# Performance work log

Measured on AMD Instinct MI355X. Metric: run time of the kernel, lower is better.

Reference implementation:

```python
import jax, jax.numpy as jnp
import numpy as np

B, N, D = 8, 2048, 256      # batch, tokens, model dim (= out_token_dims)
S = 128                     # query_key_dims
H = int(2.0 * D)            # expansion_factor * D = 512
EPS = 1e-5


def setup_inputs() -> dict:
    key = jax.random.key(0)
    ks = jax.random.split(key, 4)
    x = jax.random.normal(ks[0], (B, N, D), dtype=jnp.float32)
    g = jnp.ones((), jnp.float32)                                # ScaleNorm gain
    W_uv = jax.random.normal(ks[1], (D, 2 * H + S), jnp.float32) * 0.02
    b_uv = jnp.zeros((2 * H + S,), jnp.float32)
    gamma = jnp.ones((2, S), jnp.float32)                        # OffsetScale scale
    beta = jnp.zeros((2, S), jnp.float32)                        # OffsetScale offset
    W_o = jax.random.normal(ks[2], (H, D), jnp.float32) * 0.02
    b_o = jnp.zeros((D,), jnp.float32)
    return {"x": x, "g": g, "W_uv": W_uv, "b_uv": b_uv,
            "gamma": gamma, "beta": beta, "W_o": W_o, "b_o": b_o}


def reference(x, g, W_uv, b_uv, gamma, beta, W_o, b_o):
    d = x.shape[-1]
    # ScaleNorm: x / max(||x|| / sqrt(d), eps) * g
    norm = jnp.linalg.norm(x, axis=-1, keepdims=True) * jax.lax.rsqrt(jnp.float32(d))
    xn = x / jnp.maximum(norm, EPS) * g
    # fused uv projection + SiLU
    uv = jax.nn.silu(jnp.einsum('bnd,de->bne', xn, W_uv) + b_uv)
    u = uv[..., :H]            # gate branch        [B,N,H]
    v = uv[..., H:2 * H]       # value branch       [B,N,H]
    base = uv[..., 2 * H:]     # shared q/k base    [B,N,S]
    # OffsetScale heads=2 -> q, k (cheap per-dim affine)
    q = base * gamma[0] + beta[0]
    k = base * gamma[1] + beta[1]
    # single-head scores + ReLU^2 attention activation
    qk = jnp.einsum('bns,bms->bnm', q, k) * jax.lax.rsqrt(jnp.float32(S))
    attn = jnp.square(jax.nn.relu(qk))
    # gate * (attn @ v), then output projection back to D
    gated = u * jnp.einsum('bnm,bmh->bnh', attn, v)
    return jnp.einsum('bnh,hd->bnd', gated, W_o) + b_o
```

## Files before the change

### kernel.cpp

```cpp
#include <hip/hip_runtime.h>
#include <math.h>

#define BB 8
#define NN 2048
#define DD 256
#define SS 128
#define HH 512
#define EE 1152

typedef short bf16x8 __attribute__((ext_vector_type(8)));
typedef float f32x4 __attribute__((ext_vector_type(4)));

__device__ __forceinline__ short f2bf(float f) {
    union { float f; unsigned u; } a; a.f = f;
    unsigned r = a.u + 0x7FFFu + ((a.u >> 16) & 1u);
    return (short)(r >> 16);
}
__device__ __forceinline__ float bf2f(short s) {
    union { unsigned u; float f; } a; a.u = ((unsigned)(unsigned short)s) << 16;
    return a.f;
}
__device__ __forceinline__ void gl_lds16(const short* g, short* l) {
    __builtin_amdgcn_global_load_lds(
        (const __attribute__((address_space(1))) void*)g,
        (__attribute__((address_space(3))) void*)l, 16, 0, 0);
}

__global__ __launch_bounds__(256) void k_pre(
        const float* __restrict__ x, const float* __restrict__ gp,
        short* __restrict__ xn,
        const float* __restrict__ Wuv, const float* __restrict__ Wo,
        short* __restrict__ Wuv_t, short* __restrict__ Wo_t) {
    __shared__ float tile[32][33];
    int bid = blockIdx.x;
    int t = threadIdx.x;
    if (bid < 4096) {
        int wave = t >> 6, lane = t & 63;
        long row = (long)bid * 4 + wave;
        float4 xv = ((const float4*)(x + row * DD))[lane];
        float ss = xv.x*xv.x + xv.y*xv.y + xv.z*xv.z + xv.w*xv.w;
        #pragma unroll
        for (int off = 32; off > 0; off >>= 1) ss += __shfl_down(ss, off);
        ss = __shfl(ss, 0);
        float norm = sqrtf(ss) * 0.0625f;
        float scale = gp[0] / fmaxf(norm, 1e-5f);
        short4 o;
        o.x = f2bf(xv.x * scale); o.y = f2bf(xv.y * scale);
        o.z = f2bf(xv.z * scale); o.w = f2bf(xv.w * scale);
        ((short4*)(xn + row * DD))[lane] = o;
    } else if (bid < 4384) {
        int bid2 = bid - 4096;
        int et = bid2 % 36, dt = bid2 / 36;
        #pragma unroll
        for (int i = 0; i < 4; i++) {
            int idx = t + i*256, r = idx >> 5, c = idx & 31;
            tile[r][c] = Wuv[(long)(dt*32 + r)*EE + et*32 + c];
        }
        __syncthreads();
        #pragma unroll
        for (int i = 0; i < 4; i++) {
            int idx = t + i*256, r = idx >> 5, c = idx & 31;
            Wuv_t[(long)(et*32 + r)*DD + dt*32 + c] = f2bf(tile[c][r]);
        }
    } else {
        int bid3 = bid - 4384;
        int ht = bid3 % 16, dt = bid3 / 16;
        #pragma unroll
        for (int i = 0; i < 4; i++) {
            int idx = t + i*256, r = idx >> 5, c = idx & 31;
            tile[r][c] = Wo[(long)(ht*32 + r)*DD + dt*32 + c];
        }
        __syncthreads();
        #pragma unroll
        for (int i = 0; i < 4; i++) {
            int idx = t + i*256, r = idx >> 5, c = idx & 31;
            Wo_t[(long)(dt*32 + r)*HH + ht*32 + c] = f2bf(tile[c][r]);
        }
    }
}

__global__ __launch_bounds__(256) void k_gemm1(
        const short* __restrict__ xn, const short* __restrict__ Wuv_t,
        const float* __restrict__ b_uv,
        const float* __restrict__ gamma, const float* __restrict__ beta,
        short* __restrict__ u, short* __restrict__ vfrag,
        short* __restrict__ q, short* __restrict__ k) {
    __shared__ short As[128*64];
    __shared__ short Bs[128*64];
    int m0 = blockIdx.x * 128, n0 = blockIdx.y * 128;
    int t = threadIdx.x, w = t >> 6, lane = t & 63;
    int wr = w & 1, wc = w >> 1, l16 = lane & 15, quad = lane >> 4;
    int lr = lane >> 3, lc = (lane & 7) * 8;
    f32x4 acc[4][4] = {};
    for (int k0 = 0; k0 < DD; k0 += 64) {
        __syncthreads();
        #pragma unroll
        for (int i = 0; i < 4; i++) {
            int r0 = i*32 + w*8;
            gl_lds16(&xn[(long)(m0 + r0 + lr)*DD + k0 + lc], &As[r0*64]);
            gl_lds16(&Wuv_t[(long)(n0 + r0 + lr)*DD + k0 + lc], &Bs[r0*64]);
        }
        __syncthreads();
        #pragma unroll
        for (int kk = 0; kk < 2; kk++) {
            bf16x8 a[4], bb[4];
            #pragma unroll
            for (int mt = 0; mt < 4; mt++)
                a[mt] = *(const bf16x8*)&As[(wr*64 + mt*16 + l16)*64 + kk*32 + quad*8];
            #pragma unroll
            for (int nt = 0; nt < 4; nt++)
                bb[nt] = *(const bf16x8*)&Bs[(wc*64 + nt*16 + l16)*64 + kk*32 + quad*8];
            #pragma unroll
            for (int mt = 0; mt < 4; mt++)
                #pragma unroll
                for (int nt = 0; nt < 4; nt++)
                    acc[mt][nt] = __builtin_amdgcn_mfma_f32_16x16x32_bf16(
                        a[mt], bb[nt], acc[mt][nt], 0,0,0);
        }
    }
    #pragma unroll
    for (int mt = 0; mt < 4; mt++)
    #pragma unroll
    for (int nt = 0; nt < 4; nt++) {
        int gm0 = m0 + wr*64 + mt*16 + quad*4;
        int ge  = n0 + wc*64 + nt*16 + l16;
        float val[4];
        #pragma unroll
        for (int r = 0; r < 4; r++) {
            float xv = acc[mt][nt][r] + b_uv[ge];
            val[r] = xv / (1.0f + __expf(-xv));
        }
        if (ge < HH) {
            #pragma unroll
            for (int r = 0; r < 4; r++)
                u[(long)(gm0 + r)*HH + ge] = f2bf(val[r]);
        } else if (ge < 2*HH) {
            int h = ge - HH;
            long base = (((long)((gm0 >> 11)*64 + ((gm0 & 2047) >> 5)) * 32)
                         + (h >> 4)) * 512
                        + ((((gm0 & 31) >> 3)*16 + (h & 15)) * 8) + (gm0 & 7);
            short4 o;
            o.x = f2bf(val[0]); o.y = f2bf(val[1]);
            o.z = f2bf(val[2]); o.w = f2bf(val[3]);
            *(short4*)&vfrag[base] = o;
        } else {
            int si = ge - 2*HH;
            #pragma unroll
            for (int r = 0; r < 4; r++) {
                q[(long)(gm0 + r)*SS + si] = f2bf(val[r] * gamma[si]      + beta[si]);
                k[(long)(gm0 + r)*SS + si] = f2bf(val[r] * gamma[SS + si] + beta[SS + si]);
            }
        }
    }
}

#define KS(p,row)  (smem + ((p)*32 + (row))*136)
#define PS(p,row)  (smem + 8704 + ((p)*64 + (row))*40)
#define GT(hf,row) (smem + (hf)*16896 + (row)*264)

__global__ __launch_bounds__(512, 2) void k_attn(
        const short* __restrict__ q, const short* __restrict__ k,
        const short* __restrict__ vfrag, const short* __restrict__ u,
        const short* __restrict__ Wo_t, const float* __restrict__ b_o,
        float* __restrict__ out) {
    extern __shared__ __align__(16) short smem[];
    int b = blockIdx.x & 7;
    int i0 = (blockIdx.x >> 3) * 64;
    int t = threadIdx.x, w = t >> 6, lane = t & 63;
    int l16 = lane & 15, quad = lane >> 4;
    int qt = w >> 1, mt = w & 1;
    const short* qb  = q + ((long)b * NN + i0) * SS;
    const short* kb  = k + (long)b * NN * SS;
    const short* vfb = vfrag + (long)b * 64 * 32 * 512;
    const float RS = 0.08838834764831845f;

    int krow = t >> 4, kch = (t & 15) * 8;

    bf16x8 qf[4];
    #pragma unroll
    for (int kc = 0; kc < 4; kc++)
        qf[kc] = *(const bf16x8*)&qb[(long)(qt*16 + l16)*SS + kc*32 + quad*8];

    *(bf16x8*)&KS(0,krow)[kch] = *(const bf16x8*)&kb[(long)krow*SS + kch];
    bf16x8 kpre = *(const bf16x8*)&kb[(long)(32 + krow)*SS + kch];
    __syncthreads();

    f32x4 acc[16] = {};
    for (int it = 0; it < NN/32; it++) {
        int p = it & 1;
        int m0 = it * 32;
        int mnext = (m0 + 64 < NN) ? m0 + 64 : m0;
        bf16x8 knext = *(const bf16x8*)&kb[(long)(mnext + krow)*SS + kch];
        bf16x8 vf[4];
        #pragma unroll
        for (int jj = 0; jj < 4; jj++)
            vf[jj] = *(const bf16x8*)&vfb[((long)it*32 + (w*4 + jj))*512 + lane*8];
        f32x4 sc = {};
        #pragma unroll
        for (int kc = 0; kc < 4; kc++) {
            bf16x8 kf = *(const bf16x8*)&KS(p, mt*16 + l16)[kc*32 + quad*8];
            sc = __builtin_amdgcn_mfma_f32_16x16x32_bf16(kf, qf[kc], sc, 0,0,0);
        }
        short4 pw;
        {
            float s0 = fmaxf(sc[0]*RS, 0.f), s1 = fmaxf(sc[1]*RS, 0.f);
            float s2 = fmaxf(sc[2]*RS, 0.f), s3 = fmaxf(sc[3]*RS, 0.f);
            pw.x = f2bf(s0*s0); pw.y = f2bf(s1*s1);
            pw.z = f2bf(s2*s2); pw.w = f2bf(s3*s3);
        }
        *(short4*)&PS(p, qt*16 + l16)[mt*16 + quad*4] = pw;
        *(bf16x8*)&KS(p^1, krow)[kch] = kpre;
        kpre = knext;
        __syncthreads();
        bf16x8 af[4];
        #pragma unroll
        for (int qq2 = 0; qq2 < 4; qq2++)
            af[qq2] = *(const bf16x8*)&PS(p, qq2*16 + l16)[quad*8];
        #pragma unroll
        for (int jj = 0; jj < 4; jj++)
            #pragma unroll
            for (int qq2 = 0; qq2 < 4; qq2++)
                acc[qq2*4 + jj] = __builtin_amdgcn_mfma_f32_16x16x32_bf16(
                    af[qq2], vf[jj], acc[qq2*4 + jj], 0,0,0);
    }

    long rowbase = (long)b * NN + i0;
    __syncthreads();
    {
        int hf = w >> 2;
        int hbase = (w & 3) * 64;
        #pragma unroll
        for (int qq2 = 0; qq2 < 4; qq2++)
        #pragma unroll
        for (int jj = 0; jj < 4; jj++) {
            int gh = w*64 + jj*16 + l16;
            #pragma unroll
            for (int r = 0; r < 4; r++) {
                long grow = rowbase + qq2*16 + quad*4 + r;
                float uval = bf2f(u[grow*HH + gh]);
                GT(hf, qq2*16 + quad*4 + r)[hbase + jj*16 + l16] =
                    f2bf(acc[qq2*4 + jj][r] * uval);
            }
        }
    }
    __syncthreads();
    f32x4 acc2[4][2] = {};
    #pragma unroll
    for (int p = 0; p < 2; p++) {
        #pragma unroll
        for (int kc = 0; kc < 8; kc++) {
            bf16x8 A[4], Bf[2];
            #pragma unroll
            for (int mt2 = 0; mt2 < 4; mt2++)
                A[mt2] = *(const bf16x8*)&GT(p, mt2*16 + l16)[kc*32 + quad*8];
            #pragma unroll
            for (int nt = 0; nt < 2; nt++)
                Bf[nt] = *(const bf16x8*)&Wo_t[(long)(w*32 + nt*16 + l16)*HH
                                               + p*256 + kc*32 + quad*8];
            #pragma unroll
            for (int mt2 = 0; mt2 < 4; mt2++)
                #pragma unroll
                for (int nt = 0; nt < 2; nt++)
                    acc2[mt2][nt] = __builtin_amdgcn_mfma_f32_16x16x32_bf16(
                        A[mt2], Bf[nt], acc2[mt2][nt], 0,0,0);
        }
    }
    #pragma unroll
    for (int mt2 = 0; mt2 < 4; mt2++)
    #pragma unroll
    for (int nt = 0; nt < 2; nt++)
    #pragma unroll
    for (int r = 0; r < 4; r++) {
        long grow = rowbase + mt2*16 + quad*4 + r;
        int gd = w*32 + nt*16 + l16;
        out[grow*DD + gd] = acc2[mt2][nt][r] + b_o[gd];
    }
}

extern "C" void kernel_launch(void* const* d_in, const int* in_sizes, int n_in,
                              void* d_out, int out_size, void* d_ws, size_t ws_size,
                              hipStream_t stream) {
    const float* x     = (const float*)d_in[0];
    const float* g     = (const float*)d_in[1];
    const float* Wuv   = (const float*)d_in[2];
    const float* b_uv  = (const float*)d_in[3];
    const float* gamma = (const float*)d_in[4];
    const float* beta  = (const float*)d_in[5];
    const float* Wo    = (const float*)d_in[6];
    const float* b_o   = (const float*)d_in[7];
    float* out = (float*)d_out;

    short* ws    = (short*)d_ws;
    short* xn    = ws;
    short* Wuv_t = xn    + (long)16384 * 256;
    short* Wo_t  = Wuv_t + (long)1152 * 256;
    short* u     = Wo_t  + (long)256 * 512;
    short* vfrag = u     + (long)16384 * 512;
    short* qq    = vfrag + (long)16384 * 512;
    short* kk    = qq    + (long)16384 * 128;

    k_pre<<<4512, 256, 0, stream>>>(x, g, xn, Wuv, Wo, Wuv_t, Wo_t);
    k_gemm1<<<dim3(128, 9), 256, 0, stream>>>(xn, Wuv_t, b_uv, gamma, beta,
                                              u, vfrag, qq, kk);
    k_attn<<<256, 512, 67584, stream>>>(qq, kk, vfrag, u, Wo_t, b_o, out);
}
```

Measured before the change: 163.7 us.

## Register-prefetch GEMM1 tiles and deepen attention K/V prefetch pipeline

GEMM1 now loads its A/B tiles with register prefetch: the next k-slice is fetched into registers while MFMAs run on the current one, replacing direct global-to-LDS loads. It also adds a launch-bounds occupancy hint. The attention loop is unrolled by two with ping-pong K buffers, and V fragments are loaded one stage earlier so global latency overlaps the MFMA work. The cost is higher register pressure, which could lower occupancy or cause spills.

```diff
diff --git a/kernel.cpp b/kernel.cpp
--- a/kernel.cpp
+++ b/kernel.cpp
@@ -19,11 +19,6 @@
 __device__ __forceinline__ float bf2f(short s) {
     union { unsigned u; float f; } a; a.u = ((unsigned)(unsigned short)s) << 16;
     return a.f;
-}
-__device__ __forceinline__ void gl_lds16(const short* g, short* l) {
-    __builtin_amdgcn_global_load_lds(
-        (const __attribute__((address_space(1))) void*)g,
-        (__attribute__((address_space(3))) void*)l, 16, 0, 0);
 }
 
 __global__ __launch_bounds__(256) void k_pre(
@@ -79,7 +74,7 @@
     }
 }
 
-__global__ __launch_bounds__(256) void k_gemm1(
+__global__ __launch_bounds__(256, 3) void k_gemm1(
         const short* __restrict__ xn, const short* __restrict__ Wuv_t,
         const float* __restrict__ b_uv,
         const float* __restrict__ gamma, const float* __restrict__ beta,
@@ -90,17 +85,29 @@
     int m0 = blockIdx.x * 128, n0 = blockIdx.y * 128;
     int t = threadIdx.x, w = t >> 6, lane = t & 63;
     int wr = w & 1, wc = w >> 1, l16 = lane & 15, quad = lane >> 4;
-    int lr = lane >> 3, lc = (lane & 7) * 8;
+    int srow = t >> 1, scol = (t & 1) * 32;
     f32x4 acc[4][4] = {};
-    for (int k0 = 0; k0 < DD; k0 += 64) {
+    bf16x8 aS[4], bS[4];
+    #pragma unroll
+    for (int j = 0; j < 4; j++) {
+        aS[j] = *(const bf16x8*)&xn[(long)(m0 + srow)*DD + scol + j*8];
+        bS[j] = *(const bf16x8*)&Wuv_t[(long)(n0 + srow)*DD + scol + j*8];
+    }
+    for (int ki = 0; ki < 4; ki++) {
+        #pragma unroll
+        for (int j = 0; j < 4; j++) {
+            *(bf16x8*)&As[srow*64 + scol + j*8] = aS[j];
+            *(bf16x8*)&Bs[srow*64 + scol + j*8] = bS[j];
+        }
         __syncthreads();
-        #pragma unroll
-        for (int i = 0; i < 4; i++) {
-            int r0 = i*32 + w*8;
-            gl_lds16(&xn[(long)(m0 + r0 + lr)*DD + k0 + lc], &As[r0*64]);
-            gl_lds16(&Wuv_t[(long)(n0 + r0 + lr)*DD + k0 + lc], &Bs[r0*64]);
-        }
-        __syncthreads();
+        if (ki < 3) {
+            int k0 = (ki + 1) * 64;
+            #pragma unroll
+            for (int j = 0; j < 4; j++) {
+                aS[j] = *(const bf16x8*)&xn[(long)(m0 + srow)*DD + k0 + scol + j*8];
+                bS[j] = *(const bf16x8*)&Wuv_t[(long)(n0 + srow)*DD + k0 + scol + j*8];
+            }
+        }
         #pragma unroll
         for (int kk = 0; kk < 2; kk++) {
             bf16x8 a[4], bb[4];
@@ -117,6 +124,7 @@
                     acc[mt][nt] = __builtin_amdgcn_mfma_f32_16x16x32_bf16(
                         a[mt], bb[nt], acc[mt][nt], 0,0,0);
         }
+        __syncthreads();
     }
     #pragma unroll
     for (int mt = 0; mt < 4; mt++)
@@ -182,46 +190,79 @@
         qf[kc] = *(const bf16x8*)&qb[(long)(qt*16 + l16)*SS + kc*32 + quad*8];
 
     *(bf16x8*)&KS(0,krow)[kch] = *(const bf16x8*)&kb[(long)krow*SS + kch];
-    bf16x8 kpre = *(const bf16x8*)&kb[(long)(32 + krow)*SS + kch];
+    bf16x8 kregB = *(const bf16x8*)&kb[(long)(32 + krow)*SS + kch];
+    bf16x8 kregA = *(const bf16x8*)&kb[(long)(64 + krow)*SS + kch];
+    bf16x8 vfA[4], vfB[4];
+    #pragma unroll
+    for (int jj = 0; jj < 4; jj++)
+        vfA[jj] = *(const bf16x8*)&vfb[((long)(w*4 + jj))*512 + lane*8];
     __syncthreads();
 
     f32x4 acc[16] = {};
-    for (int it = 0; it < NN/32; it++) {
-        int p = it & 1;
-        int m0 = it * 32;
-        int mnext = (m0 + 64 < NN) ? m0 + 64 : m0;
-        bf16x8 knext = *(const bf16x8*)&kb[(long)(mnext + krow)*SS + kch];
-        bf16x8 vf[4];
-        #pragma unroll
-        for (int jj = 0; jj < 4; jj++)
-            vf[jj] = *(const bf16x8*)&vfb[((long)it*32 + (w*4 + jj))*512 + lane*8];
-        f32x4 sc = {};
-        #pragma unroll
-        for (int kc = 0; kc < 4; kc++) {
-            bf16x8 kf = *(const bf16x8*)&KS(p, mt*16 + l16)[kc*32 + quad*8];
-            sc = __builtin_amdgcn_mfma_f32_16x16x32_bf16(kf, qf[kc], sc, 0,0,0);
-        }
-        short4 pw;
+    for (int s = 0; s < 32; s++) {
         {
+            f32x4 sc = {};
+            #pragma unroll
+            for (int kc = 0; kc < 4; kc++) {
+                bf16x8 kf = *(const bf16x8*)&KS(0, mt*16 + l16)[kc*32 + quad*8];
+                sc = __builtin_amdgcn_mfma_f32_16x16x32_bf16(kf, qf[kc], sc, 0,0,0);
+            }
+            short4 pw;
             float s0 = fmaxf(sc[0]*RS, 0.f), s1 = fmaxf(sc[1]*RS, 0.f);
             float s2 = fmaxf(sc[2]*RS, 0.f), s3 = fmaxf(sc[3]*RS, 0.f);
             pw.x = f2bf(s0*s0); pw.y = f2bf(s1*s1);
             pw.z = f2bf(s2*s2); pw.w = f2bf(s3*s3);
-        }
-        *(short4*)&PS(p, qt*16 + l16)[mt*16 + quad*4] = pw;
-        *(bf16x8*)&KS(p^1, krow)[kch] = kpre;
-        kpre = knext;
-        __syncthreads();
-        bf16x8 af[4];
-        #pragma unroll
-        for (int qq2 = 0; qq2 < 4; qq2++)
-            af[qq2] = *(const bf16x8*)&PS(p, qq2*16 + l16)[quad*8];
-        #pragma unroll
-        for (int jj = 0; jj < 4; jj++)
+            *(short4*)&PS(0, qt*16 + l16)[mt*16 + quad*4] = pw;
+            *(bf16x8*)&KS(1, krow)[kch] = kregB;
+            __syncthreads();
+            int tk = (2*s + 3 < 64) ? 2*s + 3 : 63;
+            kregB = *(const bf16x8*)&kb[(long)(tk*32 + krow)*SS + kch];
+            #pragma unroll
+            for (int jj = 0; jj < 4; jj++)
+                vfB[jj] = *(const bf16x8*)&vfb[((long)(2*s+1)*32 + w*4 + jj)*512 + lane*8];
+            bf16x8 af[4];
             #pragma unroll
             for (int qq2 = 0; qq2 < 4; qq2++)
-                acc[qq2*4 + jj] = __builtin_amdgcn_mfma_f32_16x16x32_bf16(
-                    af[qq2], vf[jj], acc[qq2*4 + jj], 0,0,0);
+                af[qq2] = *(const bf16x8*)&PS(0, qq2*16 + l16)[quad*8];
+            #pragma unroll
+            for (int jj = 0; jj < 4; jj++)
+                #pragma unroll
+                for (int qq2 = 0; qq2 < 4; qq2++)
+                    acc[qq2*4 + jj] = __builtin_amdgcn_mfma_f32_16x16x32_bf16(
+                        af[qq2], vfA[jj], acc[qq2*4 + jj], 0,0,0);
+        }
+        {
+            f32x4 sc = {};
+            #pragma unroll
+            for (int kc = 0; kc < 4; kc++) {
+                bf16x8 kf = *(const bf16x8*)&KS(1, mt*16 + l16)[kc*32 + quad*8];
+                sc = __builtin_amdgcn_mfma_f32_16x16x32_bf16(kf, qf[kc], sc, 0,0,0);
+            }
+            short4 pw;
+            float s0 = fmaxf(sc[0]*RS, 0.f), s1 = fmaxf(sc[1]*RS, 0.f);
+            float s2 = fmaxf(sc[2]*RS, 0.f), s3 = fmaxf(sc[3]*RS, 0.f);
+            pw.x = f2bf(s0*s0); pw.y = f2bf(s1*s1);
+            pw.z = f2bf(s2*s2); pw.w = f2bf(s3*s3);
+            *(short4*)&PS(1, qt*16 + l16)[mt*16 + quad*4] = pw;
+            *(bf16x8*)&KS(0, krow)[kch] = kregA;
+            __syncthreads();
+            int tk = (2*s + 4 < 64) ? 2*s + 4 : 63;
+            kregA = *(const bf16x8*)&kb[(long)(tk*32 + krow)*SS + kch];
+            int tv = (2*s + 2 < 64) ? 2*s + 2 : 63;
+            #pragma unroll
+            for (int jj = 0; jj < 4; jj++)
+                vfA[jj] = *(const bf16x8*)&vfb[((long)tv*32 + w*4 + jj)*512 + lane*8];
+            bf16x8 af[4];
+            #pragma unroll
+            for (int qq2 = 0; qq2 < 4; qq2++)
+                af[qq2] = *(const bf16x8*)&PS(1, qq2*16 + l16)[quad*8];
+            #pragma unroll
+            for (int jj = 0; jj < 4; jj++)
+                #pragma unroll
+                for (int qq2 = 0; qq2 < 4; qq2++)
+                    acc[qq2*4 + jj] = __builtin_amdgcn_mfma_f32_16x16x32_bf16(
+                        af[qq2], vfB[jj], acc[qq2*4 + jj], 0,0,0);
+        }
     }
 
     long rowbase = (long)b * NN + i0;
```

Result: slower. 172.2 us (+5.2%).
